# Performance work log

Hardware: AMD Instinct MI355X
Metric: run time of the kernel (lower is better)

## Reference

```python
import jax, jax.numpy as jnp
import numpy as np

D_MODEL = 512
D_AUX = 64
B, E = 8, 2048


def setup_inputs() -> dict:
    key = jax.random.key(0)
    ks = jax.random.split(key, 12)
    x = jax.random.normal(ks[0], (B, E, D_MODEL), dtype=jnp.float32)
    query_aux = jax.random.normal(ks[1], (B, E, D_AUX), dtype=jnp.float32)
    key_aux = jax.random.normal(ks[2], (B, E, D_AUX), dtype=jnp.float32)
    adjacency_mask = jax.random.randint(ks[3], (B, E, E), 0, 2, dtype=jnp.int32)
    merge_coefficients = jax.random.uniform(ks[4], (B, E, E), dtype=jnp.float32)
    # learned parameters of IrregularityAwareAttention (nn.Linear weights stored
    # as (out, in) in torch; we keep (in, out) for x @ W)
    s = 1.0 / np.sqrt(D_MODEL)
    Wq = jax.random.uniform(ks[5], (D_MODEL, D_MODEL), minval=-s, maxval=s, dtype=jnp.float32)
    bq = jax.random.uniform(ks[6], (D_MODEL,), minval=-s, maxval=s, dtype=jnp.float32)
    Wk = jax.random.uniform(ks[7], (D_MODEL, D_MODEL), minval=-s, maxval=s, dtype=jnp.float32)
    bk = jax.random.uniform(ks[8], (D_MODEL,), minval=-s, maxval=s, dtype=jnp.float32)
    Wv = jax.random.uniform(ks[9], (D_MODEL, D_MODEL), minval=-s, maxval=s, dtype=jnp.float32)
    bv = jax.random.uniform(ks[10], (D_MODEL,), minval=-s, maxval=s, dtype=jnp.float32)
    threshold = jnp.float32(0.5)
    return {
        "x": x, "query_aux": query_aux, "key_aux": key_aux,
        "adjacency_mask": adjacency_mask, "merge_coefficients": merge_coefficients,
        "Wq": Wq, "bq": bq, "Wk": Wk, "bk": bk, "Wv": Wv, "bv": bv,
        "threshold": threshold,
    }


def reference(x, query_aux, key_aux, adjacency_mask, merge_coefficients,
              Wq, bq, Wk, bk, Wv, bv, threshold):
    d_model = x.shape[-1]
    scale = jnp.asarray(d_model, x.dtype) ** 0.5
    q = x @ Wq + bq                      # (B, E, D)
    k = x @ Wk + bk
    v = x @ Wv + bv
    scores = jnp.einsum("bed,bfd->bef", q, k) / scale   # (B, E, E)

    aux_scale = jnp.asarray(key_aux.shape[-1], x.dtype) ** 0.5
    scores_aux = jnp.einsum("bed,bfd->bef", query_aux, key_aux) / aux_scale

    non_zero_mask = scores_aux != 0
    positive_mask = scores > threshold
    merge_mask = positive_mask & non_zero_mask
    blended = (1.0 - merge_coefficients) * scores + merge_coefficients * scores_aux
    scores = jnp.where(merge_mask, blended, scores)

    mask_value = jnp.finfo(scores.dtype).min
    scores = jnp.where(adjacency_mask == 0, mask_value, scores)

    attn = jax.nn.softmax(scores, axis=-1)
    return jnp.einsum("bef,bfd->bed", attn, v)
```

## Files before the change

### kernel.cpp

```cpp
#include <hip/hip_runtime.h>

#define E2 2048
#define DM 512

typedef __attribute__((ext_vector_type(8))) _Float16 half8;
typedef __attribute__((ext_vector_type(4))) _Float16 half4;
typedef __attribute__((ext_vector_type(8))) short short8;
typedef __attribute__((ext_vector_type(4))) short shortx4;
typedef __attribute__((ext_vector_type(4))) float floatx4;

__device__ __forceinline__ void stage_tile8(const _Float16* __restrict__ g, int stride,
                                            _Float16* lds, int tid) {
  const int r0 = tid >> 2;
  const int cs = ((tid & 3) ^ (r0 & 3)) * 8;
  const int wbase = (tid >> 6) * 512;
  const _Float16* gp = g + (size_t)r0 * stride + cs;
  __builtin_amdgcn_global_load_lds(
      (const __attribute__((address_space(1))) unsigned int*)gp,
      (__attribute__((address_space(3))) unsigned int*)(lds + wbase), 16, 0, 0);
}

__device__ __forceinline__ void mfma8(const _Float16* As, const _Float16* Bs,
                                      floatx4 acc[4][2], int wm, int wn, int lane) {
  const int m16 = lane & 15, quad = lane >> 4;
  const int sq = (quad ^ (m16 & 3)) * 8;
  half8 a[4];
#pragma unroll
  for (int i = 0; i < 4; ++i)
    a[i] = *(const half8*)(As + (wm * 64 + i * 16 + m16) * 32 + sq);
#pragma unroll
  for (int j = 0; j < 2; ++j) {
    const half8 b = *(const half8*)(Bs + (wn * 32 + j * 16 + m16) * 32 + sq);
#pragma unroll
    for (int i = 0; i < 4; ++i)
      acc[i][j] = __builtin_amdgcn_mfma_f32_16x16x32_f16(a[i], b, acc[i][j], 0, 0, 0);
  }
}

__device__ __forceinline__ void mfma24(const _Float16* Ah, const _Float16* Al,
                                       const _Float16* Bh, const _Float16* Bl,
                                       floatx4 acc[4][2], int wm, int wn, int lane) {
  const int m16 = lane & 15, quad = lane >> 4;
  const int sq = (quad ^ (m16 & 3)) * 8;
  half8 ah[4], al[4];
#pragma unroll
  for (int i = 0; i < 4; ++i) {
    const int off = (wm * 64 + i * 16 + m16) * 32 + sq;
    ah[i] = *(const half8*)(Ah + off);
    al[i] = *(const half8*)(Al + off);
  }
#pragma unroll
  for (int j = 0; j < 2; ++j) {
    const int off = (wn * 32 + j * 16 + m16) * 32 + sq;
    const half8 bh = *(const half8*)(Bh + off);
    const half8 bl = *(const half8*)(Bl + off);
#pragma unroll
    for (int i = 0; i < 4; ++i) {
      acc[i][j] = __builtin_amdgcn_mfma_f32_16x16x32_f16(ah[i], bh, acc[i][j], 0, 0, 0);
      acc[i][j] = __builtin_amdgcn_mfma_f32_16x16x32_f16(al[i], bh, acc[i][j], 0, 0, 0);
      acc[i][j] = __builtin_amdgcn_mfma_f32_16x16x32_f16(ah[i], bl, acc[i][j], 0, 0, 0);
    }
  }
}

__global__ void split_conv_k(const float* __restrict__ src, _Float16* __restrict__ hi,
                             _Float16* __restrict__ lo, float scale, int n8) {
  int i = blockIdx.x * blockDim.x + threadIdx.x;
  const int stride = gridDim.x * blockDim.x;
  const float4* s4 = (const float4*)src;
  for (; i < n8; i += stride) {
    const float4 u = s4[2 * i], v = s4[2 * i + 1];
    const float g[8] = {u.x, u.y, u.z, u.w, v.x, v.y, v.z, v.w};
    half8 h, l;
#pragma unroll
    for (int t = 0; t < 8; ++t) {
      const float gv = g[t] * scale;
      const _Float16 hv = (_Float16)gv;
      h[t] = hv;
      l[t] = (_Float16)(gv - (float)hv);
    }
    ((half8*)hi)[i] = h;
    ((half8*)lo)[i] = l;
  }
}

__global__ void conv_k(const float* __restrict__ src, _Float16* __restrict__ dst, int n8) {
  int i = blockIdx.x * blockDim.x + threadIdx.x;
  const int stride = gridDim.x * blockDim.x;
  const float4* s4 = (const float4*)src;
  for (; i < n8; i += stride) {
    const float4 u = s4[2 * i], v = s4[2 * i + 1];
    const float g[8] = {u.x, u.y, u.z, u.w, v.x, v.y, v.z, v.w};
    half8 h;
#pragma unroll
    for (int t = 0; t < 8; ++t) h[t] = (_Float16)g[t];
    ((half8*)dst)[i] = h;
  }
}

__global__ void transw_k(const float* __restrict__ Wq, const float* __restrict__ Wk,
                         const float* __restrict__ Wv, _Float16* __restrict__ Wth,
                         _Float16* __restrict__ Wtl) {
  const int z = blockIdx.z;
  const float* W = (z == 0) ? Wq : (z == 1) ? Wk : Wv;
  __shared__ float t[32][33];
  const int n0 = blockIdx.x * 32, k0 = blockIdx.y * 32;
  const int tx = threadIdx.x, ty = threadIdx.y;
#pragma unroll
  for (int i = 0; i < 32; i += 8) t[ty + i][tx] = W[(size_t)(k0 + ty + i) * DM + n0 + tx];
  __syncthreads();
  const size_t zb = (size_t)z * DM * DM;
#pragma unroll
  for (int i = 0; i < 32; i += 8) {
    const float g = t[tx][ty + i] * 64.0f;
    const _Float16 h = (_Float16)g;
    const size_t o = zb + (size_t)(n0 + ty + i) * DM + (k0 + tx);
    Wth[o] = h;
    Wtl[o] = (_Float16)(g - (float)h);
  }
}

__global__ __launch_bounds__(512, 4) void qkv_k(
    const _Float16* __restrict__ xh, const _Float16* __restrict__ xl,
    const _Float16* __restrict__ Wth, const _Float16* __restrict__ Wtl,
    const float* __restrict__ bqp, const float* __restrict__ bkp,
    const float* __restrict__ bvp,
    _Float16* __restrict__ qh, _Float16* __restrict__ ql,
    _Float16* __restrict__ kh, _Float16* __restrict__ kl,
    _Float16* __restrict__ vT) {
  __shared__ _Float16 Ah[2][4096], Al[2][4096], Bh[2][4096], Bl[2][4096];
  const int tid = threadIdx.x, lane = tid & 63, wv = tid >> 6;
  const int wm = wv >> 2, wn = wv & 3;
  const int flat = blockIdx.x + 128 * blockIdx.y + 512 * blockIdx.z;
  const int virt = (flat & 7) * 192 + (flat >> 3);
  const int bm = virt & 127, bn = (virt >> 7) & 3, z = virt >> 9;
  const bool split = (z < 2);
  const _Float16* Ash = xh + (size_t)bm * 128 * DM;
  const _Float16* Asl = xl + (size_t)bm * 128 * DM;
  const _Float16* Bsh = Wth + ((size_t)z * DM + bn * 128) * DM;
  const _Float16* Bsl = Wtl + ((size_t)z * DM + bn * 128) * DM;
  floatx4 acc[4][2];
  const floatx4 z4 = {0.f, 0.f, 0.f, 0.f};
#pragma unroll
  for (int i = 0; i < 4; ++i)
#pragma unroll
    for (int j = 0; j < 2; ++j) acc[i][j] = z4;

  stage_tile8(Ash, DM, Ah[0], tid);
  stage_tile8(Bsh, DM, Bh[0], tid);
  if (split) { stage_tile8(Asl, DM, Al[0], tid); stage_tile8(Bsl, DM, Bl[0], tid); }
  __syncthreads();
  for (int kt = 0; kt < 16; ++kt) {
    const int cur = kt & 1, nxt = cur ^ 1;
    if (kt < 15) {
      const int ko = (kt + 1) * 32;
      stage_tile8(Ash + ko, DM, Ah[nxt], tid);
      stage_tile8(Bsh + ko, DM, Bh[nxt], tid);
      if (split) { stage_tile8(Asl + ko, DM, Al[nxt], tid); stage_tile8(Bsl + ko, DM, Bl[nxt], tid); }
    }
    if (split) mfma24(Ah[cur], Al[cur], Bh[cur], Bl[cur], acc, wm, wn, lane);
    else       mfma8(Ah[cur], Bh[cur], acc, wm, wn, lane);
    __syncthreads();
  }
  const int m16 = lane & 15, quad = lane >> 4;
  const float* bias = (z == 0) ? bqp : (z == 1) ? bkp : bvp;
  if (split) {
    _Float16* oh = (z == 0) ? qh : kh;
    _Float16* ol = (z == 0) ? ql : kl;
#pragma unroll
    for (int j = 0; j < 2; ++j) {
      const int n = bn * 128 + wn * 32 + j * 16 + m16;
      const float bb = bias[n];
#pragma unroll
      for (int i = 0; i < 4; ++i) {
        const int m = bm * 128 + wm * 64 + i * 16 + quad * 4;
#pragma unroll
        for (int r = 0; r < 4; ++r) {
          const float val = acc[i][j][r] * (1.0f / 256.0f) + bb;
          const float v8 = val * 8.0f;
          const _Float16 h = (_Float16)v8;
          const _Float16 l = (_Float16)(v8 - (float)h);
          const size_t o = (size_t)(m + r) * DM + n;
          oh[o] = h; ol[o] = l;
        }
      }
    }
  } else {
#pragma unroll
    for (int j = 0; j < 2; ++j) {
      const int n = bn * 128 + wn * 32 + j * 16 + m16;
      const float bb = bias[n];
#pragma unroll
      for (int i = 0; i < 4; ++i) {
        const int m = bm * 128 + wm * 64 + i * 16 + quad * 4;
        const int bidx = m >> 11, e0 = m & 2047;
        half4 pk;
#pragma unroll
        for (int r = 0; r < 4; ++r)
          pk[r] = (_Float16)(acc[i][j][r] * (1.0f / 256.0f) + bb);
        *(half4*)(vT + ((size_t)bidx * DM + n) * E2 + e0) = pk;
      }
    }
  }
}

__global__ __launch_bounds__(512, 4) void scores_k(
    const _Float16* __restrict__ qh, const _Float16* __restrict__ ql,
    const _Float16* __restrict__ kh, const _Float16* __restrict__ kl,
    const _Float16* __restrict__ qah, const _Float16* __restrict__ kah,
    const float* __restrict__ mc,
    const float* __restrict__ thrp, unsigned short* __restrict__ sc) {
  __shared__ _Float16 S[32768];
  _Float16* const AhB = S;
  _Float16* const AlB = S + 8192;
  _Float16* const BhB = S + 16384;
  _Float16* const BlB = S + 24576;
  const int tid = threadIdx.x, lane = tid & 63, wv = tid >> 6;
  const int wm = wv >> 2, wn = wv & 3;
  const int flat = blockIdx.x + 16 * blockIdx.y + 256 * blockIdx.z;
  const int virt = (flat & 7) * 256 + (flat >> 3);
  const int bf = virt & 15, be = (virt >> 4) & 15, b = virt >> 8;
  const _Float16* Ash = qh + ((size_t)b * E2 + be * 128) * DM;
  const _Float16* Asl = ql + ((size_t)b * E2 + be * 128) * DM;
  const _Float16* Bsh = kh + ((size_t)b * E2 + bf * 128) * DM;
  const _Float16* Bsl = kl + ((size_t)b * E2 + bf * 128) * DM;
  floatx4 accm[4][2];
  const floatx4 z4 = {0.f, 0.f, 0.f, 0.f};
#pragma unroll
  for (int i = 0; i < 4; ++i)
#pragma unroll
    for (int j = 0; j < 2; ++j) accm[i][j] = z4;

  stage_tile8(Ash, DM, AhB, tid);
  stage_tile8(Bsh, DM, BhB, tid);
  stage_tile8(Asl, DM, AlB, tid);
  stage_tile8(Bsl, DM, BlB, tid);
  __syncthreads();
  for (int kt = 0; kt < 16; ++kt) {
    const int cur = kt & 1, nxt = cur ^ 1;
    if (kt < 15) {
      const int ko = (kt + 1) * 32;
      stage_tile8(Ash + ko, DM, AhB + nxt * 4096, tid);
      stage_tile8(Bsh + ko, DM, BhB + nxt * 4096, tid);
      stage_tile8(Asl + ko, DM, AlB + nxt * 4096, tid);
      stage_tile8(Bsl + ko, DM, BlB + nxt * 4096, tid);
    }
    mfma24(AhB + cur * 4096, AlB + cur * 4096, BhB + cur * 4096, BlB + cur * 4096,
           accm, wm, wn, lane);
    __syncthreads();
  }
  floatx4 acca[4][2];
#pragma unroll
  for (int i = 0; i < 4; ++i)
#pragma unroll
    for (int j = 0; j < 2; ++j) acca[i][j] = z4;
  const _Float16* A2 = qah + ((size_t)b * E2 + be * 128) * 64;
  const _Float16* B2 = kah + ((size_t)b * E2 + bf * 128) * 64;
  stage_tile8(A2, 64, AhB, tid);
  stage_tile8(B2, 64, BhB, tid);
  stage_tile8(A2 + 32, 64, AhB + 4096, tid);
  stage_tile8(B2 + 32, 64, BhB + 4096, tid);
  __syncthreads();
  mfma8(AhB, BhB, acca, wm, wn, lane);
  mfma8(AhB + 4096, BhB + 4096, acca, wm, wn, lane);

  float* const sL = (float*)S;
  _Float16* const saL = S + 16896;
  const float thr = *thrp;
  const int m16 = lane & 15, quad = lane >> 4;
  const size_t rowbase0 = (size_t)b * E2 + be * 128;
#pragma unroll
  for (int h = 0; h < 2; ++h) {
    __syncthreads();
    if (wm == h) {
#pragma unroll
      for (int j = 0; j < 2; ++j) {
        const int cl = wn * 32 + j * 16 + m16;
#pragma unroll
        for (int i = 0; i < 4; ++i) {
#pragma unroll
          for (int r = 0; r < 4; ++r) {
            const int rl = i * 16 + quad * 4 + r;
            sL[rl * 132 + cl] = accm[i][j][r] * (0.015625f * 0.044194173824159216f);
            saL[rl * 132 + cl] = (_Float16)(acca[i][j][r] * 0.125f);
          }
        }
      }
    }
    __syncthreads();
#pragma unroll
    for (int g = 0; g < 4; ++g) {
      const int tf = g * 2048 + tid * 4;
      const int rl = tf >> 7, cl = tf & 127;
      const size_t idx = (rowbase0 + h * 64 + rl) * E2 + bf * 128 + cl;
      const float4 c4 = *(const float4*)(mc + idx);
      const float4 s4v = *(const float4*)(sL + rl * 132 + cl);
      const half4 sa4 = *(const half4*)(saL + rl * 132 + cl);
      const float ss[4] = {s4v.x, s4v.y, s4v.z, s4v.w};
      const float cc[4] = {c4.x, c4.y, c4.z, c4.w};
      shortx4 o;
#pragma unroll
      for (int t = 0; t < 4; ++t) {
        float s = ss[t];
        const float sa = (float)sa4[t];
        if (sa != 0.0f && s > thr) s = (1.0f - cc[t]) * s + cc[t] * sa;
        union { _Float16 hh; unsigned short u; } u;
        u.hh = (_Float16)s;
        o[t] = (short)u.u;
      }
      *(shortx4*)(sc + idx) = o;
    }
  }
}

__global__ __launch_bounds__(256) void smax_k(unsigned short* __restrict__ sc,
                                              const int* __restrict__ adj) {
  const size_t row = blockIdx.x;
  unsigned short* p = sc + row * E2;
  const int* arow = adj + row * E2;
  const int tid = threadIdx.x, lane = tid & 63, wv = tid >> 6;
  const short8 raw = *(const short8*)(p + tid * 8);
  const int4 a0 = *(const int4*)(arow + tid * 8);
  const int4 a1 = *(const int4*)(arow + tid * 8 + 4);
  const int aa[8] = {a0.x, a0.y, a0.z, a0.w, a1.x, a1.y, a1.z, a1.w};
  float f[8];
#pragma unroll
  for (int t = 0; t < 8; ++t) {
    union { _Float16 h; short s; } u; u.s = raw[t];
    f[t] = aa[t] ? (float)u.h : -65504.0f;
  }
  float mx = f[0];
#pragma unroll
  for (int t = 1; t < 8; ++t) mx = fmaxf(mx, f[t]);
#pragma unroll
  for (int o = 32; o > 0; o >>= 1) mx = fmaxf(mx, __shfl_xor(mx, o, 64));
  __shared__ float red[8];
  if (lane == 0) red[wv] = mx;
  __syncthreads();
  mx = fmaxf(fmaxf(red[0], red[1]), fmaxf(red[2], red[3]));
  float ef[8], sum = 0.f;
#pragma unroll
  for (int t = 0; t < 8; ++t) { ef[t] = __expf(f[t] - mx); sum += ef[t]; }
#pragma unroll
  for (int o = 32; o > 0; o >>= 1) sum += __shfl_xor(sum, o, 64);
  if (lane == 0) red[4 + wv] = sum;
  __syncthreads();
  sum = (red[4] + red[5]) + (red[6] + red[7]);
  const float inv = 1.0f / sum;
  short8 ov;
#pragma unroll
  for (int t = 0; t < 8; ++t) {
    union { _Float16 h; short s; } u;
    u.h = (_Float16)(ef[t] * inv);
    ov[t] = u.s;
  }
  *(short8*)(p + tid * 8) = ov;
}

__global__ __launch_bounds__(512, 6) void pv_k(
    const _Float16* __restrict__ at, const _Float16* __restrict__ vT,
    float* __restrict__ out) {
  __shared__ _Float16 As[2][4096], Bs[2][4096];
  const int tid = threadIdx.x, lane = tid & 63, wv = tid >> 6;
  const int wm = wv >> 2, wn = wv & 3;
  const int flat = blockIdx.x + 4 * blockIdx.y + 64 * blockIdx.z;
  const int virt = (flat & 7) * 64 + (flat >> 3);
  const int bd = virt & 3, be = (virt >> 2) & 15, b = virt >> 6;
  const _Float16* Asrc = at + ((size_t)b * E2 + be * 128) * E2;
  const _Float16* Bsrc = vT + ((size_t)b * DM + bd * 128) * E2;
  floatx4 acc[4][2];
  const floatx4 z4 = {0.f, 0.f, 0.f, 0.f};
#pragma unroll
  for (int i = 0; i < 4; ++i)
#pragma unroll
    for (int j = 0; j < 2; ++j) acc[i][j] = z4;
  stage_tile8(Asrc, E2, As[0], tid);
  stage_tile8(Bsrc, E2, Bs[0], tid);
  __syncthreads();
  for (int kt = 0; kt < 64; ++kt) {
    const int cur = kt & 1, nxt = cur ^ 1;
    if (kt < 63) {
      const int ko = (kt + 1) * 32;
      stage_tile8(Asrc + ko, E2, As[nxt], tid);
      stage_tile8(Bsrc + ko, E2, Bs[nxt], tid);
    }
    mfma8(As[cur], Bs[cur], acc, wm, wn, lane);
    __syncthreads();
  }
  const int m16 = lane & 15, quad = lane >> 4;
#pragma unroll
  for (int j = 0; j < 2; ++j) {
    const int d = bd * 128 + wn * 32 + j * 16 + m16;
#pragma unroll
    for (int i = 0; i < 4; ++i) {
      const int e0 = be * 128 + wm * 64 + i * 16 + quad * 4;
#pragma unroll
      for (int r = 0; r < 4; ++r)
        out[((size_t)b * E2 + e0 + r) * DM + d] = acc[i][j][r];
    }
  }
}

extern "C" void kernel_launch(void* const* d_in, const int* in_sizes, int n_in,
                              void* d_out, int out_size, void* d_ws, size_t ws_size,
                              hipStream_t stream) {
  const float* x   = (const float*)d_in[0];
  const float* qa  = (const float*)d_in[1];
  const float* ka  = (const float*)d_in[2];
  const int*   adj = (const int*)d_in[3];
  const float* mc  = (const float*)d_in[4];
  const float* Wq  = (const float*)d_in[5];
  const float* bq  = (const float*)d_in[6];
  const float* Wk  = (const float*)d_in[7];
  const float* bk  = (const float*)d_in[8];
  const float* Wv  = (const float*)d_in[9];
  const float* bv  = (const float*)d_in[10];
  const float* thr = (const float*)d_in[11];
  float* out = (float*)d_out;
  char* w = (char*)d_ws;
  const size_t MiB = 1ull << 20;
  _Float16* xh  = (_Float16*)(w + 0 * MiB);
  _Float16* xl  = (_Float16*)(w + 16 * MiB);
  _Float16* qhp = (_Float16*)(w + 32 * MiB);
  _Float16* qlp = (_Float16*)(w + 48 * MiB);
  _Float16* khp = (_Float16*)(w + 64 * MiB);
  _Float16* klp = (_Float16*)(w + 80 * MiB);
  _Float16* vT  = (_Float16*)(w + 96 * MiB);
  _Float16* Wth = (_Float16*)(w + 112 * MiB);
  _Float16* Wtl = (_Float16*)(w + 114 * MiB);
  _Float16* qah = (_Float16*)(w + 116 * MiB);
  _Float16* kah = (_Float16*)(w + 118 * MiB);
  unsigned short* sc = (unsigned short*)(w + 120 * MiB);

  split_conv_k<<<2048, 256, 0, stream>>>(x, xh, xl, 4.0f, (8 * E2 * DM) / 8);
  conv_k<<<256, 256, 0, stream>>>(qa, qah, (8 * E2 * 64) / 8);
  conv_k<<<256, 256, 0, stream>>>(ka, kah, (8 * E2 * 64) / 8);
  transw_k<<<dim3(16, 16, 3), dim3(32, 8), 0, stream>>>(Wq, Wk, Wv, Wth, Wtl);
  qkv_k<<<dim3(128, 4, 3), 512, 0, stream>>>(xh, xl, Wth, Wtl, bq, bk, bv,
                                             qhp, qlp, khp, klp, vT);
  scores_k<<<dim3(16, 16, 8), 512, 0, stream>>>(qhp, qlp, khp, klp, qah, kah,
                                                mc, thr, sc);
  smax_k<<<16384, 256, 0, stream>>>(sc, adj);
  pv_k<<<dim3(4, 16, 8), 512, 0, stream>>>((const _Float16*)sc, vT, out);
}
```

Measured before the change: 589.9 us.

## Replace syncthreads with partial vmcnt waits and triple-buffer PV loads

In the qkv and scores GEMM loops, the full __syncthreads is replaced by explicit s_waitcnt vmcnt(N) so the next tile's global-to-LDS loads can stay in flight while the current tile computes, with raw barriers and sched_barriers around the MFMA block. The pv kernel moves to a triple LDS buffer, which lets it drop the trailing barrier each iteration. Block-index swizzles also change: qkv uses a new remap and scores drops its swizzle for a plain grid mapping. The hand-written waitcnt counts rely on the exact number of outstanding loads and on compiler scheduling, so a wrong count would be a correctness risk, and the extra pv LDS may lower occupancy.

```diff
diff --git a/kernel.cpp b/kernel.cpp
--- a/kernel.cpp
+++ b/kernel.cpp
@@ -8,6 +8,13 @@
 typedef __attribute__((ext_vector_type(8))) short short8;
 typedef __attribute__((ext_vector_type(4))) short shortx4;
 typedef __attribute__((ext_vector_type(4))) float floatx4;
+
+#define WAITV4 asm volatile("s_waitcnt vmcnt(4)" ::: "memory")
+#define WAITV2 asm volatile("s_waitcnt vmcnt(2)" ::: "memory")
+#define WAITV0 asm volatile("s_waitcnt vmcnt(0)" ::: "memory")
+#define WAITL0 asm volatile("s_waitcnt lgkmcnt(0)" ::: "memory")
+#define BARRIER __builtin_amdgcn_s_barrier()
+#define SCHEDB __builtin_amdgcn_sched_barrier(0)
 
 __device__ __forceinline__ void stage_tile8(const _Float16* __restrict__ g, int stride,
                                             _Float16* lds, int tid) {
@@ -131,9 +138,11 @@
   __shared__ _Float16 Ah[2][4096], Al[2][4096], Bh[2][4096], Bl[2][4096];
   const int tid = threadIdx.x, lane = tid & 63, wv = tid >> 6;
   const int wm = wv >> 2, wn = wv & 3;
-  const int flat = blockIdx.x + 128 * blockIdx.y + 512 * blockIdx.z;
-  const int virt = (flat & 7) * 192 + (flat >> 3);
-  const int bm = virt & 127, bn = (virt >> 7) & 3, z = virt >> 9;
+  const int flat = blockIdx.x + 128 * (blockIdx.y + 4 * blockIdx.z);
+  const int s = flat & 7, k = flat >> 3;
+  const int bm = s * 16 + (k & 15);
+  const int bnz = k >> 4;
+  const int bn = bnz & 3, z = bnz >> 2;
   const bool split = (z < 2);
   const _Float16* Ash = xh + (size_t)bm * 128 * DM;
   const _Float16* Asl = xl + (size_t)bm * 128 * DM;
@@ -149,18 +158,29 @@
   stage_tile8(Ash, DM, Ah[0], tid);
   stage_tile8(Bsh, DM, Bh[0], tid);
   if (split) { stage_tile8(Asl, DM, Al[0], tid); stage_tile8(Bsl, DM, Bl[0], tid); }
-  __syncthreads();
   for (int kt = 0; kt < 16; ++kt) {
     const int cur = kt & 1, nxt = cur ^ 1;
     if (kt < 15) {
       const int ko = (kt + 1) * 32;
       stage_tile8(Ash + ko, DM, Ah[nxt], tid);
       stage_tile8(Bsh + ko, DM, Bh[nxt], tid);
-      if (split) { stage_tile8(Asl + ko, DM, Al[nxt], tid); stage_tile8(Bsl + ko, DM, Bl[nxt], tid); }
-    }
+      if (split) {
+        stage_tile8(Asl + ko, DM, Al[nxt], tid);
+        stage_tile8(Bsl + ko, DM, Bl[nxt], tid);
+        WAITV4;
+      } else {
+        WAITV2;
+      }
+    } else {
+      WAITV0;
+    }
+    BARRIER;
+    SCHEDB;
     if (split) mfma24(Ah[cur], Al[cur], Bh[cur], Bl[cur], acc, wm, wn, lane);
     else       mfma8(Ah[cur], Bh[cur], acc, wm, wn, lane);
-    __syncthreads();
+    WAITL0;
+    BARRIER;
+    SCHEDB;
   }
   const int m16 = lane & 15, quad = lane >> 4;
   const float* bias = (z == 0) ? bqp : (z == 1) ? bkp : bvp;
@@ -217,9 +237,7 @@
   _Float16* const BlB = S + 24576;
   const int tid = threadIdx.x, lane = tid & 63, wv = tid >> 6;
   const int wm = wv >> 2, wn = wv & 3;
-  const int flat = blockIdx.x + 16 * blockIdx.y + 256 * blockIdx.z;
-  const int virt = (flat & 7) * 256 + (flat >> 3);
-  const int bf = virt & 15, be = (virt >> 4) & 15, b = virt >> 8;
+  const int bf = blockIdx.x, be = blockIdx.y, b = blockIdx.z;
   const _Float16* Ash = qh + ((size_t)b * E2 + be * 128) * DM;
   const _Float16* Asl = ql + ((size_t)b * E2 + be * 128) * DM;
   const _Float16* Bsh = kh + ((size_t)b * E2 + bf * 128) * DM;
@@ -235,7 +253,6 @@
   stage_tile8(Bsh, DM, BhB, tid);
   stage_tile8(Asl, DM, AlB, tid);
   stage_tile8(Bsl, DM, BlB, tid);
-  __syncthreads();
   for (int kt = 0; kt < 16; ++kt) {
     const int cur = kt & 1, nxt = cur ^ 1;
     if (kt < 15) {
@@ -244,10 +261,17 @@
       stage_tile8(Bsh + ko, DM, BhB + nxt * 4096, tid);
       stage_tile8(Asl + ko, DM, AlB + nxt * 4096, tid);
       stage_tile8(Bsl + ko, DM, BlB + nxt * 4096, tid);
-    }
+      WAITV4;
+    } else {
+      WAITV0;
+    }
+    BARRIER;
+    SCHEDB;
     mfma24(AhB + cur * 4096, AlB + cur * 4096, BhB + cur * 4096, BlB + cur * 4096,
            accm, wm, wn, lane);
-    __syncthreads();
+    WAITL0;
+    BARRIER;
+    SCHEDB;
   }
   floatx4 acca[4][2];
 #pragma unroll
@@ -360,7 +384,7 @@
 __global__ __launch_bounds__(512, 6) void pv_k(
     const _Float16* __restrict__ at, const _Float16* __restrict__ vT,
     float* __restrict__ out) {
-  __shared__ _Float16 As[2][4096], Bs[2][4096];
+  __shared__ _Float16 As[3][4096], Bs[3][4096];
   const int tid = threadIdx.x, lane = tid & 63, wv = tid >> 6;
   const int wm = wv >> 2, wn = wv & 3;
   const int flat = blockIdx.x + 4 * blockIdx.y + 64 * blockIdx.z;
@@ -376,16 +400,22 @@
     for (int j = 0; j < 2; ++j) acc[i][j] = z4;
   stage_tile8(Asrc, E2, As[0], tid);
   stage_tile8(Bsrc, E2, Bs[0], tid);
-  __syncthreads();
+  int cur = 0;
   for (int kt = 0; kt < 64; ++kt) {
-    const int cur = kt & 1, nxt = cur ^ 1;
+    const int nxt = (cur == 2) ? 0 : cur + 1;
     if (kt < 63) {
       const int ko = (kt + 1) * 32;
       stage_tile8(Asrc + ko, E2, As[nxt], tid);
       stage_tile8(Bsrc + ko, E2, Bs[nxt], tid);
-    }
+      WAITV2;
+    } else {
+      WAITV0;
+    }
+    BARRIER;
+    SCHEDB;
     mfma8(As[cur], Bs[cur], acc, wm, wn, lane);
-    __syncthreads();
+    WAITL0;
+    cur = nxt;
   }
   const int m16 = lane & 15, quad = lane >> 4;
 #pragma unroll
```

After: 564.1 us. 1.05x faster.
